# Kernel tuning notes

Measured on AMD Instinct MI355X. Metric: run time of the kernel, lower is better.

## Reference

```python
import jax, jax.numpy as jnp
import numpy as np
import math

BATCH, SEQLEN, DMODEL, NSTATE, DFF = 4, 2048, 1024, 16, 4096
EPS = 1e-6


def rmsnorm(x, scale):
    return x * jax.lax.rsqrt(jnp.mean(x * x, axis=-1, keepdims=True) + EPS) * scale


def ssm_scan(u, A_ssm, B_ssm, C_ssm, D_ssm):
    # u: (B, L, D). Diagonal SSM per (d, n) channel/state pair.
    dt = jnp.exp(jnp.linspace(math.log(0.001), math.log(0.1), NSTATE))  # (N,)
    expA = jnp.exp(A_ssm)                 # (D, N); continuous A = -expA
    dA = jnp.exp(-expA * dt)              # (D, N) discrete decay
    dB = B_ssm * (1.0 - dA) / expA        # (D, N) ZOH input matrix

    def step(s, u_t):
        # s: (B, D, N), u_t: (B, D)
        s = s * dA + u_t[..., None] * dB
        y = jnp.einsum('bdn,dn->bd', s, C_ssm)
        return s, y

    s0 = jnp.zeros((u.shape[0], DMODEL, NSTATE), dtype=u.dtype)
    _, ys = jax.lax.scan(step, s0, jnp.transpose(u, (1, 0, 2)))  # ys: (L, B, D)
    return jnp.transpose(ys, (1, 0, 2)) + u * D_ssm


def setup_inputs() -> dict:
    key = jax.random.key(0)
    ks = jax.random.split(key, 6)
    return {
        'x': jax.random.normal(ks[0], (BATCH, SEQLEN, DMODEL), jnp.float32),
        'A_ssm': jax.random.normal(ks[1], (DMODEL, NSTATE), jnp.float32),
        'B_ssm': jax.random.normal(ks[2], (DMODEL, NSTATE), jnp.float32),
        'C_ssm': jax.random.normal(ks[3], (DMODEL, NSTATE), jnp.float32),
        'D_ssm': jnp.zeros((DMODEL,), jnp.float32),
        'scale1': jnp.ones((DMODEL,), jnp.float32),
        'scale2': jnp.ones((DMODEL,), jnp.float32),
        'w1': jax.random.normal(ks[4], (DMODEL, DFF), jnp.float32) * 0.02,
        'b1': jnp.zeros((DFF,), jnp.float32),
        'w2': jax.random.normal(ks[5], (DFF, DMODEL), jnp.float32) * 0.02,
        'b2': jnp.zeros((DMODEL,), jnp.float32),
    }


def reference(x, A_ssm, B_ssm, C_ssm, D_ssm, scale1, scale2, w1, b1, w2, b2):
    x = x + ssm_scan(rmsnorm(x, scale1), A_ssm, B_ssm, C_ssm, D_ssm)
    h = rmsnorm(x, scale2)
    h = jax.nn.gelu(h @ w1 + b1, approximate=False) @ w2 + b2
    return x + h
```

## Files before the change

### kernel.cpp

```cpp
#include <hip/hip_runtime.h>
#include <cstdint>
#include <cstddef>


#define BATCH 4
#define SEQLEN 2048
#define DMODEL 1024
#define NSTATE 16
#define DFF 4096
#define NCH 32
#define LCH 64

typedef unsigned short ushort_t;
typedef __attribute__((ext_vector_type(8))) short short8;
typedef __attribute__((ext_vector_type(4))) float f32x4;

__device__ __forceinline__ ushort_t f2bf(float f) {
  uint32_t u = __builtin_bit_cast(uint32_t, f);
  uint32_t r = (u + 0x7FFFu + ((u >> 16) & 1u)) >> 16;
  return (ushort_t)r;
}

__global__ void coef_kernel(const float* __restrict__ A_ssm, const float* __restrict__ B_ssm,
                            const float* __restrict__ C_ssm,
                            float* __restrict__ dA_t, float* __restrict__ dBz_t,
                            float* __restrict__ dAc_t, float* __restrict__ Ct) {
  int d = blockIdx.x * 256 + threadIdx.x;
  if (d >= DMODEL) return;
  const float l0 = -6.907755278982137f;
  const float ld = 0.30701134573253947f;
  for (int n = 0; n < NSTATE; n++) {
    float dt = expf(l0 + (float)n * ld);
    float a  = A_ssm[d * NSTATE + n];
    float ea = expf(a);
    float da = expf(-ea * dt);
    float dbz = B_ssm[d * NSTATE + n] * (1.f - da) / ea;
    float dac = expf(-ea * dt * (float)LCH);
    dA_t [n * DMODEL + d] = da;
    dBz_t[n * DMODEL + d] = dbz;
    dAc_t[n * DMODEL + d] = dac;
    Ct   [n * DMODEL + d] = C_ssm[d * NSTATE + n];
  }
}

__global__ void transpose_to_bf16(const float* __restrict__ src, ushort_t* __restrict__ dst,
                                  int R, int C) {
  __shared__ float tile[32][33];
  int bx = blockIdx.x * 32, by = blockIdx.y * 32;
  int tx = threadIdx.x, ty = threadIdx.y;
  #pragma unroll
  for (int i = 0; i < 4; i++) {
    int r = by + ty + i * 8;
    tile[ty + i * 8][tx] = src[(size_t)r * C + bx + tx];
  }
  __syncthreads();
  #pragma unroll
  for (int i = 0; i < 4; i++) {
    int c = bx + ty + i * 8;
    dst[(size_t)c * R + by + tx] = f2bf(tile[tx][ty + i * 8]);
  }
}

__global__ void rms1_kernel(const float* __restrict__ x, float* __restrict__ rrms) {
  int row = blockIdx.x * 4 + (threadIdx.x >> 6);
  int lane = threadIdx.x & 63;
  const float4* p = (const float4*)(x + (size_t)row * DMODEL);
  float s = 0.f;
  #pragma unroll
  for (int w = 0; w < 4; w++) {
    float4 v = p[w * 64 + lane];
    s += v.x * v.x + v.y * v.y + v.z * v.z + v.w * v.w;
  }
  #pragma unroll
  for (int off = 32; off; off >>= 1) s += __shfl_xor(s, off, 64);
  if (lane == 0) rrms[row] = rsqrtf(s * (1.f / DMODEL) + 1e-6f);
}

__global__ void scan_pass1(const float* __restrict__ x, const float* __restrict__ rrms,
                           const float* __restrict__ scale1,
                           const float* __restrict__ dA_t, const float* __restrict__ dBz_t,
                           float* __restrict__ s_fin) {
  int d = blockIdx.x * 256 + threadIdx.x;
  int b = blockIdx.y, c = blockIdx.z;
  float dA[NSTATE], dBz[NSTATE], s[NSTATE];
  #pragma unroll
  for (int n = 0; n < NSTATE; n++) {
    dA[n] = dA_t[n * DMODEL + d];
    dBz[n] = dBz_t[n * DMODEL + d];
    s[n] = 0.f;
  }
  float sc1 = scale1[d];
  const float* xp = x + ((size_t)b * SEQLEN + (size_t)c * LCH) * DMODEL + d;
  const float* rp = rrms + b * SEQLEN + c * LCH;
  for (int t = 0; t < LCH; t++) {
    float u = xp[(size_t)t * DMODEL] * rp[t] * sc1;
    #pragma unroll
    for (int n = 0; n < NSTATE; n++) s[n] = fmaf(s[n], dA[n], u * dBz[n]);
  }
  #pragma unroll
  for (int n = 0; n < NSTATE; n++)
    s_fin[(((size_t)n * BATCH + b) * NCH + c) * DMODEL + d] = s[n];
}

__global__ void scan_pass2(const float* __restrict__ s_fin, const float* __restrict__ dAc_t,
                           float* __restrict__ s_in) {
  int idx = blockIdx.x * 256 + threadIdx.x;
  int d = idx & (DMODEL - 1);
  int b = (idx >> 10) & (BATCH - 1);
  int n = idx >> 12;
  float dc = dAc_t[n * DMODEL + d];
  float s = 0.f;
  for (int c = 0; c < NCH; c++) {
    size_t o = (((size_t)n * BATCH + b) * NCH + c) * DMODEL + d;
    s_in[o] = s;
    s = s_fin[o] + dc * s;
  }
}

__global__ void scan_pass3(const float* __restrict__ x, const float* __restrict__ rrms,
                           const float* __restrict__ scale1,
                           const float* __restrict__ dA_t, const float* __restrict__ dBz_t,
                           const float* __restrict__ Ct, const float* __restrict__ Dv,
                           const float* __restrict__ s_in, float* __restrict__ out) {
  int d = blockIdx.x * 256 + threadIdx.x;
  int b = blockIdx.y, c = blockIdx.z;
  float dA[NSTATE], dBz[NSTATE], Cc[NSTATE], s[NSTATE];
  #pragma unroll
  for (int n = 0; n < NSTATE; n++) {
    dA[n] = dA_t[n * DMODEL + d];
    dBz[n] = dBz_t[n * DMODEL + d];
    Cc[n] = Ct[n * DMODEL + d];
    s[n] = s_in[(((size_t)n * BATCH + b) * NCH + c) * DMODEL + d];
  }
  float sc1 = scale1[d], Dd = Dv[d];
  const float* xp = x + ((size_t)b * SEQLEN + (size_t)c * LCH) * DMODEL + d;
  const float* rp = rrms + b * SEQLEN + c * LCH;
  float* op = out + ((size_t)b * SEQLEN + (size_t)c * LCH) * DMODEL + d;
  for (int t = 0; t < LCH; t++) {
    float xv = xp[(size_t)t * DMODEL];
    float u = xv * rp[t] * sc1;
    float y = 0.f;
    #pragma unroll
    for (int n = 0; n < NSTATE; n++) {
      s[n] = fmaf(s[n], dA[n], u * dBz[n]);
      y = fmaf(Cc[n], s[n], y);
    }
    op[(size_t)t * DMODEL] = xv + y + u * Dd;
  }
}

__global__ void rms2_kernel(const float* __restrict__ x2, const float* __restrict__ scale2,
                            ushort_t* __restrict__ hb) {
  int row = blockIdx.x * 4 + (threadIdx.x >> 6);
  int lane = threadIdx.x & 63;
  const float4* p = (const float4*)(x2 + (size_t)row * DMODEL);
  float4 v[4];
  float s = 0.f;
  #pragma unroll
  for (int w = 0; w < 4; w++) {
    v[w] = p[w * 64 + lane];
    s += v[w].x * v[w].x + v[w].y * v[w].y + v[w].z * v[w].z + v[w].w * v[w].w;
  }
  #pragma unroll
  for (int off = 32; off; off >>= 1) s += __shfl_xor(s, off, 64);
  float r = rsqrtf(s * (1.f / DMODEL) + 1e-6f);
  const float4* sc = (const float4*)scale2;
  #pragma unroll
  for (int w = 0; w < 4; w++) {
    float4 scv = sc[w * 64 + lane];
    ushort4 u;
    u.x = f2bf(v[w].x * r * scv.x);
    u.y = f2bf(v[w].y * r * scv.y);
    u.z = f2bf(v[w].z * r * scv.z);
    u.w = f2bf(v[w].w * r * scv.w);
    *(ushort4*)(hb + (size_t)row * DMODEL + (size_t)(w * 64 + lane) * 4) = u;
  }
}


template <int N>
__device__ __forceinline__ void fence_vm() {
  asm volatile("s_waitcnt vmcnt(%0)" :: "n"(N) : "memory");
}

__device__ __forceinline__ void bar() { asm volatile("s_barrier" ::: "memory"); }

__device__ __forceinline__ void gl2lds16(const ushort_t* g, ushort_t* l) {
  __builtin_amdgcn_global_load_lds(
      (const __attribute__((address_space(1))) unsigned int*)g,
      (__attribute__((address_space(3))) unsigned int*)l, 16, 0, 0);
}

template <int K, int MODE>
__global__ __launch_bounds__(1024, 4) void gemm16v(const ushort_t* __restrict__ A,
                                                   const ushort_t* __restrict__ B,
                                                   const float* __restrict__ bias,
                                                   const float* __restrict__ resid,
                                                   void* __restrict__ outp,
                                                   int M, int N) {
  constexpr int TILEA = 16384;
  constexpr int SLOT  = TILEA + 8192;
  constexpr int NT = K / 64;
  __shared__ __align__(16) ushort_t lds[3 * SLOT];

  const int tid = threadIdx.x;
  const int wave = tid >> 6, lane = tid & 63;
  const int wr = wave >> 2, wc = wave & 3;

  const int nwg = gridDim.x, cpx = nwg >> 3, bid = blockIdx.x;
  const int wg = (bid & 7) * cpx + (bid >> 3);
  const int nbn = N / 128;
  const int m0 = (wg / nbn) * 256, n0 = (wg % nbn) * 128;

  const int scol = 8 * ((tid & 7) ^ ((tid >> 3) & 7));
  const int wo = wave * 512;

  const ushort_t* aStgLo = A + (size_t)(m0 + (tid >> 3)) * K + scol;
  const ushort_t* aStgHi = aStgLo + (size_t)128 * K;
  const ushort_t* bStg   = B + (size_t)(n0 + (tid >> 3)) * K + scol;

  f32x4 acc[4][2] = {};

  {
    ushort_t* s0p = lds;
    gl2lds16(aStgLo, s0p + wo);
    gl2lds16(aStgHi, s0p + 8192 + wo);
    gl2lds16(bStg,   s0p + TILEA + wo);
    ushort_t* s1p = lds + SLOT;
    gl2lds16(aStgLo + 64, s1p + wo);
    gl2lds16(aStgHi + 64, s1p + 8192 + wo);
    gl2lds16(bStg   + 64, s1p + TILEA + wo);
    aStgLo += 128; aStgHi += 128; bStg += 128;
  }
  fence_vm<3>(); bar();

  const int rl = lane & 15, c4 = lane >> 4;
  const int sw0 = (c4 ^ (rl & 7)) * 8;
  const int sw1 = ((4 | c4) ^ (rl & 7)) * 8;
  const int aOff = (wr * 64 + rl) * 64;
  const int bOff = TILEA + (wc * 32 + rl) * 64;

  const ushort_t* rSlot = lds;
  ushort_t*       wSlot = lds + 2 * SLOT;

  for (int t = 0; t < NT; ++t) {
    const ushort_t* ra0 = rSlot + aOff + sw0;
    const ushort_t* ra1 = rSlot + aOff + sw1;
    const ushort_t* rb0 = rSlot + bOff + sw0;
    const ushort_t* rb1 = rSlot + bOff + sw1;

    short8 af[2][4], bf[2][2];
    #pragma unroll
    for (int m = 0; m < 4; m++) {
      af[0][m] = *(const short8*)(ra0 + m * 1024);
      af[1][m] = *(const short8*)(ra1 + m * 1024);
    }
    #pragma unroll
    for (int n = 0; n < 2; n++) {
      bf[0][n] = *(const short8*)(rb0 + n * 1024);
      bf[1][n] = *(const short8*)(rb1 + n * 1024);
    }

    if (t + 2 < NT) {
      gl2lds16(aStgLo, wSlot + wo);
      gl2lds16(aStgHi, wSlot + 8192 + wo);
      gl2lds16(bStg,   wSlot + TILEA + wo);
      aStgLo += 64; aStgHi += 64; bStg += 64;
    }

    __builtin_amdgcn_s_setprio(1);
    #pragma unroll
    for (int kk = 0; kk < 2; kk++)
      #pragma unroll
      for (int m = 0; m < 4; m++)
        #pragma unroll
        for (int n = 0; n < 2; n++)
          acc[m][n] = __builtin_amdgcn_mfma_f32_16x16x32_bf16(af[kk][m], bf[kk][n],
                                                              acc[m][n], 0, 0, 0);
    __builtin_amdgcn_s_setprio(0);

    if (t + 2 < NT) fence_vm<3>();
    else            fence_vm<0>();
    bar();

    const ushort_t* rn = rSlot + SLOT;
    rSlot = (rn == lds + 3 * SLOT) ? lds : rn;
    ushort_t* wn = wSlot + SLOT;
    wSlot = (wn == lds + 3 * SLOT) ? lds : wn;
  }

  const int colb = n0 + wc * 32 + rl;
  const int rowb = m0 + wr * 64 + c4 * 4;
  #pragma unroll
  for (int n = 0; n < 2; n++) {
    int col = colb + n * 16;
    float bs = bias[col];
    #pragma unroll
    for (int m = 0; m < 4; m++) {
      int row = rowb + m * 16;
      #pragma unroll
      for (int j = 0; j < 4; j++) {
        float v = acc[m][n][j] + bs;
        size_t o = (size_t)(row + j) * N + col;
        if (MODE == 1) {
          float g = v / (1.f + __expf(-1.702f * v));
          ((ushort_t*)outp)[o] = f2bf(g);
        } else {
          ((float*)outp)[o] = resid[o] + v;
        }
      }
    }
  }
}

extern "C" void kernel_launch(void* const* d_in, const int* in_sizes, int n_in,
                              void* d_out, int out_size, void* d_ws, size_t ws_size,
                              hipStream_t stream) {
  (void)in_sizes; (void)n_in; (void)out_size; (void)ws_size;
  const float* x      = (const float*)d_in[0];
  const float* A_ssm  = (const float*)d_in[1];
  const float* B_ssm  = (const float*)d_in[2];
  const float* C_ssm  = (const float*)d_in[3];
  const float* D_ssm  = (const float*)d_in[4];
  const float* scale1 = (const float*)d_in[5];
  const float* scale2 = (const float*)d_in[6];
  const float* w1     = (const float*)d_in[7];
  const float* b1     = (const float*)d_in[8];
  const float* w2     = (const float*)d_in[9];
  const float* b2     = (const float*)d_in[10];
  float* out = (float*)d_out;

  char* ws = (char*)d_ws;
  float*    rrms  = (float*)(ws + 0);
  float*    dA_t  = (float*)(ws + 32768);
  float*    dBz_t = (float*)(ws + 98304);
  float*    dAc_t = (float*)(ws + 163840);
  float*    Ct    = (float*)(ws + 229376);
  float*    s_fin = (float*)(ws + 294912);
  float*    s_in  = (float*)(ws + 8683520);
  ushort_t* hb    = (ushort_t*)(ws + 17072128);
  ushort_t* w1t   = (ushort_t*)(ws + 33849344);
  ushort_t* w2t   = (ushort_t*)(ws + 42237952);
  ushort_t* gb    = (ushort_t*)(ws + 50626560);

  const int ROWS = BATCH * SEQLEN;

  coef_kernel<<<DMODEL / 256, 256, 0, stream>>>(A_ssm, B_ssm, C_ssm, dA_t, dBz_t, dAc_t, Ct);
  transpose_to_bf16<<<dim3(DFF / 32, DMODEL / 32), dim3(32, 8), 0, stream>>>(w1, w1t, DMODEL, DFF);
  transpose_to_bf16<<<dim3(DMODEL / 32, DFF / 32), dim3(32, 8), 0, stream>>>(w2, w2t, DFF, DMODEL);
  rms1_kernel<<<ROWS / 4, 256, 0, stream>>>(x, rrms);
  scan_pass1<<<dim3(DMODEL / 256, BATCH, NCH), 256, 0, stream>>>(x, rrms, scale1, dA_t, dBz_t, s_fin);
  scan_pass2<<<(BATCH * DMODEL * NSTATE) / 256, 256, 0, stream>>>(s_fin, dAc_t, s_in);
  scan_pass3<<<dim3(DMODEL / 256, BATCH, NCH), 256, 0, stream>>>(x, rrms, scale1, dA_t, dBz_t, Ct,
                                                                 D_ssm, s_in, out);
  rms2_kernel<<<ROWS / 4, 256, 0, stream>>>(out, scale2, hb);

  gemm16v<DMODEL, 1><<<(ROWS / 256) * (DFF / 128), 1024, 0, stream>>>(
      hb, w1t, b1, nullptr, gb, ROWS, DFF);
  gemm16v<DFF, 2><<<(ROWS / 256) * (DMODEL / 128), 1024, 0, stream>>>(
      gb, w2t, b2, out, out, ROWS, DMODEL);
}
```

Measured before the change: 224.0 us.

## Use 256x256 double-buffered tile kernel for the first FFN GEMM

Replaces the generic 256x128 triple-buffered GEMM for the up-projection with a dedicated kernel using 256x256 output tiles. Each wave computes a 64x64 sub-tile, operands stream into two LDS slots through direct global-to-LDS loads, and the LDS layout uses an XOR swizzle. Bias and a sigmoid-form GELU are fused into the bf16 store. The larger tile is meant to raise operand reuse and arithmetic intensity, at the cost of half as many workgroups and 128KB of LDS per block.

```diff
diff --git a/kernel.cpp b/kernel.cpp
--- a/kernel.cpp
+++ b/kernel.cpp
@@ -177,7 +177,6 @@
   }
 }
 
-
 template <int N>
 __device__ __forceinline__ void fence_vm() {
   asm volatile("s_waitcnt vmcnt(%0)" :: "n"(N) : "memory");
@@ -189,6 +188,119 @@
   __builtin_amdgcn_global_load_lds(
       (const __attribute__((address_space(1))) unsigned int*)g,
       (__attribute__((address_space(3))) unsigned int*)l, 16, 0, 0);
+}
+
+template <int K>
+__global__ __launch_bounds__(1024, 4) void gemm_w64(const ushort_t* __restrict__ A,
+                                                    const ushort_t* __restrict__ B,
+                                                    const float* __restrict__ bias,
+                                                    ushort_t* __restrict__ outp,
+                                                    int M, int N) {
+  constexpr int SLOT = 32768;
+  constexpr int NT = K / 64;
+  __shared__ __align__(16) ushort_t lds[2 * SLOT];
+
+  const int tid = threadIdx.x;
+  const int wave = tid >> 6, lane = tid & 63;
+  const int wr = wave >> 2, wc = wave & 3;
+
+  const int nwg = gridDim.x, cpx = nwg >> 3, bid = blockIdx.x;
+  const int wg = (bid & 7) * cpx + (bid >> 3);
+  const int nbn = N / 256;
+  const int m0 = (wg / nbn) * 256, n0 = (wg % nbn) * 256;
+
+  const int scol = 8 * ((tid & 7) ^ ((tid >> 3) & 7));
+  const int wo = wave * 512;
+  const ushort_t* aStg = A + (size_t)(m0 + (tid >> 3)) * K + scol;
+  const ushort_t* aStg2 = aStg + (size_t)128 * K;
+  const ushort_t* bStg = B + (size_t)(n0 + (tid >> 3)) * K + scol;
+  const ushort_t* bStg2 = bStg + (size_t)128 * K;
+
+  f32x4 acc[4][4] = {};
+
+  {
+    ushort_t* d = lds + wo;
+    gl2lds16(aStg,  d);
+    gl2lds16(aStg2, d + 8192);
+    gl2lds16(bStg,  d + 16384);
+    gl2lds16(bStg2, d + 24576);
+    aStg += 64; aStg2 += 64; bStg += 64; bStg2 += 64;
+  }
+  fence_vm<0>(); bar();
+
+  const int rl = lane & 15, c4 = lane >> 4;
+  const int sw0 = (c4 ^ (rl & 7)) * 8;
+  const int sw1 = ((4 | c4) ^ (rl & 7)) * 8;
+  const int aOff = (wr * 64 + rl) * 64;
+  const int bOff = 16384 + (wc * 64 + rl) * 64;
+
+  const ushort_t* rSlot = lds;
+  ushort_t*       wSlot = lds + SLOT;
+
+  for (int t = 0; t < NT; ++t) {
+    if (t + 1 < NT) {
+      gl2lds16(aStg,  wSlot + wo);
+      gl2lds16(aStg2, wSlot + 8192 + wo);
+      gl2lds16(bStg,  wSlot + 16384 + wo);
+      gl2lds16(bStg2, wSlot + 24576 + wo);
+      aStg += 64; aStg2 += 64; bStg += 64; bStg2 += 64;
+    }
+
+    const ushort_t* ra0 = rSlot + aOff + sw0;
+    const ushort_t* ra1 = rSlot + aOff + sw1;
+    const ushort_t* rb0 = rSlot + bOff + sw0;
+    const ushort_t* rb1 = rSlot + bOff + sw1;
+
+    {
+      short8 af[4], bf[4];
+      #pragma unroll
+      for (int m = 0; m < 4; m++) af[m] = *(const short8*)(ra0 + m * 1024);
+      #pragma unroll
+      for (int n = 0; n < 4; n++) bf[n] = *(const short8*)(rb0 + n * 1024);
+      __builtin_amdgcn_s_setprio(1);
+      #pragma unroll
+      for (int m = 0; m < 4; m++)
+        #pragma unroll
+        for (int n = 0; n < 4; n++)
+          acc[m][n] = __builtin_amdgcn_mfma_f32_16x16x32_bf16(af[m], bf[n], acc[m][n], 0, 0, 0);
+      __builtin_amdgcn_s_setprio(0);
+    }
+    {
+      short8 af[4], bf[4];
+      #pragma unroll
+      for (int m = 0; m < 4; m++) af[m] = *(const short8*)(ra1 + m * 1024);
+      #pragma unroll
+      for (int n = 0; n < 4; n++) bf[n] = *(const short8*)(rb1 + n * 1024);
+      __builtin_amdgcn_s_setprio(1);
+      #pragma unroll
+      for (int m = 0; m < 4; m++)
+        #pragma unroll
+        for (int n = 0; n < 4; n++)
+          acc[m][n] = __builtin_amdgcn_mfma_f32_16x16x32_bf16(af[m], bf[n], acc[m][n], 0, 0, 0);
+      __builtin_amdgcn_s_setprio(0);
+    }
+
+    if (t + 1 < NT) { fence_vm<0>(); bar(); }
+    const ushort_t* tmp = rSlot; rSlot = wSlot; wSlot = (ushort_t*)tmp;
+  }
+
+  const int colb = n0 + wc * 64 + rl;
+  const int rowb = m0 + wr * 64 + c4 * 4;
+  #pragma unroll
+  for (int n = 0; n < 4; n++) {
+    int col = colb + n * 16;
+    float bs = bias[col];
+    #pragma unroll
+    for (int m = 0; m < 4; m++) {
+      int row = rowb + m * 16;
+      #pragma unroll
+      for (int j = 0; j < 4; j++) {
+        float v = acc[m][n][j] + bs;
+        float g = v / (1.f + __expf(-1.702f * v));
+        outp[(size_t)(row + j) * N + col] = f2bf(g);
+      }
+    }
+  }
 }
 
 template <int K, int MODE>
@@ -355,8 +467,8 @@
                                                                  D_ssm, s_in, out);
   rms2_kernel<<<ROWS / 4, 256, 0, stream>>>(out, scale2, hb);
 
-  gemm16v<DMODEL, 1><<<(ROWS / 256) * (DFF / 128), 1024, 0, stream>>>(
-      hb, w1t, b1, nullptr, gb, ROWS, DFF);
+  gemm_w64<DMODEL><<<(ROWS / 256) * (DFF / 256), 1024, 0, stream>>>(
+      hb, w1t, b1, gb, ROWS, DFF);
   gemm16v<DFF, 2><<<(ROWS / 256) * (DMODEL / 128), 1024, 0, stream>>>(
       gb, w2t, b2, out, out, ROWS, DMODEL);
 }
```

Measured after the change: 211.0 us (median of 2 runs). 5.8% less time.

## Add 256x256-tile 8-wave pipelined GEMM for first FFN layer

Applied to the files above, without the earlier changes.

Replaces the first FFN GEMM with a new kernel that computes a 256x256 output tile per 512-thread workgroup. It interleaves LDS fragment reads, global-to-LDS staging and MFMA quadrants with barriers and wave priority hints, and uses a swizzled LDS layout with a remapped block order. The larger tile raises data reuse per load and aims to hide memory latency behind matrix ops, at the cost of more LDS and registers per workgroup. The epilogue applies a sigmoid-based GELU approximation.

```diff
diff --git a/kernel.cpp b/kernel.cpp
--- a/kernel.cpp
+++ b/kernel.cpp
@@ -177,7 +177,6 @@
   }
 }
 
-
 template <int N>
 __device__ __forceinline__ void fence_vm() {
   asm volatile("s_waitcnt vmcnt(%0)" :: "n"(N) : "memory");
@@ -189,6 +188,136 @@
   __builtin_amdgcn_global_load_lds(
       (const __attribute__((address_space(1))) unsigned int*)g,
       (__attribute__((address_space(3))) unsigned int*)l, 16, 0, 0);
+}
+
+#define RDA_(DST, BASE)                                                  \
+  _Pragma("unroll") for (int m_ = 0; m_ < 4; ++m_) {                     \
+    DST[0][m_] = *(const short8*)((BASE) + sw0 + m_ * 1024);             \
+    DST[1][m_] = *(const short8*)((BASE) + sw1 + m_ * 1024);             \
+  }
+#define RDB_(DST, BASE, NP)                                              \
+  _Pragma("unroll") for (int n_ = 0; n_ < 2; ++n_) {                     \
+    DST[0][n_] = *(const short8*)((BASE) + sw0 + ((NP)*2 + n_) * 1024);  \
+    DST[1][n_] = *(const short8*)((BASE) + sw1 + ((NP)*2 + n_) * 1024);  \
+  }
+#define MMAQ(S, NP, AF, BF)                                              \
+  __builtin_amdgcn_s_setprio(1);                                         \
+  _Pragma("unroll") for (int kk_ = 0; kk_ < 2; ++kk_)                    \
+  _Pragma("unroll") for (int m_ = 0; m_ < 4; ++m_)                       \
+  _Pragma("unroll") for (int n_ = 0; n_ < 2; ++n_)                       \
+    acc[(S)*4 + m_][(NP)*2 + n_] = __builtin_amdgcn_mfma_f32_16x16x32_bf16( \
+        AF[kk_][m_], BF[kk_][n_], acc[(S)*4 + m_][(NP)*2 + n_], 0, 0, 0);\
+  __builtin_amdgcn_s_setprio(0);
+
+template <int K>
+__global__ __launch_bounds__(512, 2) void gemm8f(const ushort_t* __restrict__ A,
+                                                 const ushort_t* __restrict__ B,
+                                                 const float* __restrict__ bias,
+                                                 ushort_t* __restrict__ outp,
+                                                 int M, int N) {
+  constexpr int NT = K / 64;
+  constexpr int NITER = NT / 2;
+  __shared__ __align__(16) ushort_t lds[65536];
+
+  const int tid = threadIdx.x;
+  const int wave = tid >> 6, lane = tid & 63;
+  const int wr = wave >> 2, wc = wave & 3;
+
+  const int nwg = gridDim.x, cpx = nwg >> 3, bid = blockIdx.x;
+  const int wg = (bid & 7) * cpx + (bid >> 3);
+  const int nbn = N / 256;
+  const int m0 = (wg / nbn) * 256, n0 = (wg % nbn) * 256;
+
+  const int scol = 8 * ((tid & 7) ^ ((tid >> 3) & 7));
+  const ushort_t* gA = A + (size_t)(m0 + (tid >> 3)) * K + scol;
+  const ushort_t* gB = B + (size_t)(n0 + (tid >> 3)) * K + scol;
+  const int wo = wave * 512;
+
+  auto stgA = [&](int buf, int h, int t) {
+    ushort_t* d = lds + buf * 16384 + h * 8192 + wo;
+    const ushort_t* s = gA + (size_t)(h * 128) * K + (size_t)t * 64;
+    gl2lds16(s, d);
+    gl2lds16(s + (size_t)64 * K, d + 4096);
+  };
+  auto stgB = [&](int buf, int h, int t) {
+    ushort_t* d = lds + 32768 + buf * 16384 + h * 8192 + wo;
+    const ushort_t* s = gB + (size_t)(h * 128) * K + (size_t)t * 64;
+    gl2lds16(s, d);
+    gl2lds16(s + (size_t)64 * K, d + 4096);
+  };
+
+  f32x4 acc[8][4] = {};
+
+  stgA(0, 0, 0); stgA(0, 1, 0); stgB(0, 0, 0); stgB(0, 1, 0);
+  stgA(1, 0, 1); stgA(1, 1, 1);
+  fence_vm<4>(); bar();
+
+  const int rl = lane & 15, c4 = lane >> 4;
+  const int sw0 = (c4 ^ (rl & 7)) * 8;
+  const int sw1 = ((4 | c4) ^ (rl & 7)) * 8;
+  const ushort_t* aR00 = lds + (wr * 128 + 0 * 64 + rl) * 64;
+  const ushort_t* aR01 = aR00 + 4096;
+  const ushort_t* aR10 = aR00 + 16384;
+  const ushort_t* aR11 = aR10 + 4096;
+  const ushort_t* bR0  = lds + 32768 + (wc * 64 + rl) * 64;
+  const ushort_t* bR1  = bR0 + 16384;
+
+  short8 Af0[2][4], Af1[2][4], Bf01[2][2], Bf23[2][2];
+
+  for (int i = 0; i < NITER - 1; ++i) {
+    const int t1 = 2 * i + 1, t2 = 2 * i + 2, t3 = 2 * i + 3;
+    RDA_(Af0, aR00) RDB_(Bf01, bR0, 0) stgB(1, 0, t1);
+    bar(); MMAQ(0, 0, Af0, Bf01) bar();
+    RDA_(Af1, aR01) stgB(1, 1, t1);
+    bar(); MMAQ(1, 0, Af1, Bf01) bar();
+    RDB_(Bf23, bR0, 1) stgA(0, 0, t2);
+    bar(); MMAQ(0, 1, Af0, Bf23) bar();
+    stgA(0, 1, t2); fence_vm<4>();
+    bar(); MMAQ(1, 1, Af1, Bf23) bar();
+    RDA_(Af0, aR10) RDB_(Bf01, bR1, 0) stgB(0, 0, t2);
+    bar(); MMAQ(0, 0, Af0, Bf01) bar();
+    RDA_(Af1, aR11) stgB(0, 1, t2);
+    bar(); MMAQ(1, 0, Af1, Bf01) bar();
+    RDB_(Bf23, bR1, 1) stgA(1, 0, t3);
+    bar(); MMAQ(0, 1, Af0, Bf23) bar();
+    stgA(1, 1, t3); fence_vm<4>();
+    bar(); MMAQ(1, 1, Af1, Bf23) bar();
+  }
+  {
+    RDA_(Af0, aR00) RDB_(Bf01, bR0, 0) stgB(1, 0, NT - 1);
+    bar(); MMAQ(0, 0, Af0, Bf01) bar();
+    RDA_(Af1, aR01) stgB(1, 1, NT - 1);
+    bar(); MMAQ(1, 0, Af1, Bf01) bar();
+    RDB_(Bf23, bR0, 1)
+    bar(); MMAQ(0, 1, Af0, Bf23) bar();
+    fence_vm<0>();
+    bar(); MMAQ(1, 1, Af1, Bf23) bar();
+    RDA_(Af0, aR10) RDB_(Bf01, bR1, 0)
+    bar(); MMAQ(0, 0, Af0, Bf01) bar();
+    RDA_(Af1, aR11)
+    bar(); MMAQ(1, 0, Af1, Bf01) bar();
+    RDB_(Bf23, bR1, 1)
+    bar(); MMAQ(0, 1, Af0, Bf23) bar();
+    bar(); MMAQ(1, 1, Af1, Bf23) bar();
+  }
+
+  const int colb = n0 + wc * 64 + rl;
+  const int rowb = m0 + wr * 128 + c4 * 4;
+  #pragma unroll
+  for (int n = 0; n < 4; n++) {
+    int col = colb + n * 16;
+    float bs = bias[col];
+    #pragma unroll
+    for (int mi = 0; mi < 8; mi++) {
+      int row = rowb + (mi >> 2) * 64 + (mi & 3) * 16;
+      #pragma unroll
+      for (int j = 0; j < 4; j++) {
+        float v = acc[mi][n][j] + bs;
+        float g = v / (1.f + __expf(-1.702f * v));
+        outp[(size_t)(row + j) * N + col] = f2bf(g);
+      }
+    }
+  }
 }
 
 template <int K, int MODE>
@@ -355,8 +484,8 @@
                                                                  D_ssm, s_in, out);
   rms2_kernel<<<ROWS / 4, 256, 0, stream>>>(out, scale2, hb);
 
-  gemm16v<DMODEL, 1><<<(ROWS / 256) * (DFF / 128), 1024, 0, stream>>>(
-      hb, w1t, b1, nullptr, gb, ROWS, DFF);
+  gemm8f<DMODEL><<<(ROWS / 256) * (DFF / 256), 512, 0, stream>>>(
+      hb, w1t, b1, gb, ROWS, DFF);
   gemm16v<DFF, 2><<<(ROWS / 256) * (DMODEL / 128), 1024, 0, stream>>>(
       gb, w2t, b2, out, out, ROWS, DMODEL);
 }
```

Result: faster. 212.3 us (-5.2%).
